# Optimization experiments

Hardware: AMD Instinct MI355X
Metric: run time of the kernel (lower is better)

Reference implementation:

```python
import jax, jax.numpy as jnp
import numpy as np

N_NODES = 100000
N_EDGES = 1600000
N_GRAPHS = 1000


def _gcn_layer(x, W, b, row, col, dinv):
    # GCNConv with improved=True: A_hat = A + 2I, symmetric normalization.
    xw = x @ W  # [N, out]
    norm = dinv[row] * dinv[col]  # [E]
    agg = jax.ops.segment_sum(norm[:, None] * xw[row], col, num_segments=N_NODES)
    # self-loop contribution with fill weight 2.0
    agg = agg + (2.0 * dinv * dinv)[:, None] * xw
    return agg + b


def setup_inputs() -> dict:
    key = jax.random.key(0)
    ks = jax.random.split(key, 20)
    x = jax.random.normal(ks[0], (N_NODES, 336), dtype=jnp.float32)
    edge_index = jax.random.randint(ks[1], (2, N_EDGES), 0, N_NODES, dtype=jnp.int64)
    batch = jnp.sort(jax.random.randint(ks[2], (N_NODES,), 0, N_GRAPHS, dtype=jnp.int64))
    def lin(k, din, dout):
        s = 1.0 / np.sqrt(din)
        return jax.random.uniform(k, (din, dout), jnp.float32, -s, s)
    params = {
        'W1': lin(ks[3], 336, 100), 'b1': jnp.zeros((100,), jnp.float32),
        'W2': lin(ks[4], 100, 100), 'b2': jnp.zeros((100,), jnp.float32),
        'W3': lin(ks[5], 100, 100), 'b3': jnp.zeros((100,), jnp.float32),
        'W4': lin(ks[6], 100, 100), 'b4': jnp.zeros((100,), jnp.float32),
        'W5': lin(ks[7], 100, 100), 'b5': jnp.zeros((100,), jnp.float32),
        'Wl1': lin(ks[8], 100, 100), 'bl1': jnp.zeros((100,), jnp.float32),
        'Wl2': lin(ks[9], 100, 100), 'bl2': jnp.zeros((100,), jnp.float32),
        'Wl3': lin(ks[10], 100, 29), 'bl3': jnp.zeros((29,), jnp.float32),
    }
    return {'x': x, 'edge_index': edge_index, 'batch': batch, **params}


def reference(x, edge_index, batch, W1, b1, W2, b2, W3, b3, W4, b4, W5, b5,
              Wl1, bl1, Wl2, bl2, Wl3, bl3):
    row, col = edge_index[0], edge_index[1]
    # degree of A + 2I (edge weights are 1, self-loop weight 2)
    deg = jax.ops.segment_sum(jnp.ones((N_EDGES,), x.dtype), col, num_segments=N_NODES) + 2.0
    dinv = deg ** -0.5
    h = jax.nn.relu(_gcn_layer(x, W1, b1, row, col, dinv))
    h = jax.nn.relu(_gcn_layer(h, W2, b2, row, col, dinv))
    h = jax.nn.relu(_gcn_layer(h, W3, b3, row, col, dinv))
    h = jax.nn.relu(_gcn_layer(h, W4, b4, row, col, dinv))
    h = jax.nn.relu(_gcn_layer(h, W5, b5, row, col, dinv))
    # global mean pool over graphs
    sums = jax.ops.segment_sum(h, batch, num_segments=N_GRAPHS)
    counts = jax.ops.segment_sum(jnp.ones((N_NODES,), h.dtype), batch, num_segments=N_GRAPHS)
    pooled = sums / jnp.maximum(counts, 1.0)[:, None]
    g = jax.nn.relu(pooled @ Wl1 + bl1)
    g = jax.nn.relu(g @ Wl2 + bl2)
    return g @ Wl3 + bl3
```

## Files before the change

### kernel.cpp

```cpp
#include <hip/hip_runtime.h>
#include <hip/hip_fp16.h>
#include <stdint.h>

#define NN 100000
#define NE 1600000
#define NG 1000
#define LDA 112
#define LDH 112
#define LDX 128

typedef float f32x4 __attribute__((ext_vector_type(4)));
typedef short s16x8 __attribute__((ext_vector_type(8)));

__device__ __forceinline__ unsigned short f2bf(float f) {
    unsigned u = __builtin_bit_cast(unsigned, f);
    unsigned r = u + 0x7FFFu + ((u >> 16) & 1u);
    return (unsigned short)(r >> 16);
}
__device__ __forceinline__ float bf2f(unsigned short h) {
    unsigned u = ((unsigned)h) << 16;
    return __builtin_bit_cast(float, u);
}

__global__ void k_deg(const int* __restrict__ col, int* __restrict__ degcnt) {
    int e = blockIdx.x * 256 + threadIdx.x;
    if (e < NE) atomicAdd(&degcnt[col[e]], 1);
}

__global__ void k_scan1(const int* __restrict__ cnt, int* __restrict__ csum) {
    __shared__ int s[256];
    int i = blockIdx.x * 256 + threadIdx.x;
    s[threadIdx.x] = (i < NN) ? cnt[i] : 0;
    __syncthreads();
    for (int o = 128; o > 0; o >>= 1) {
        if (threadIdx.x < o) s[threadIdx.x] += s[threadIdx.x + o];
        __syncthreads();
    }
    if (threadIdx.x == 0) csum[blockIdx.x] = s[0];
}

__global__ void k_scan2(const int* __restrict__ csum, int* __restrict__ csum2, int nb) {
    __shared__ int s[512];
    int t = threadIdx.x;
    int v = (t < nb) ? csum[t] : 0;
    s[t] = v; __syncthreads();
    for (int o = 1; o < 512; o <<= 1) {
        int x = (t >= o) ? s[t - o] : 0;
        __syncthreads();
        s[t] += x;
        __syncthreads();
    }
    if (t < nb) csum2[t] = s[t] - v;
}

__global__ void k_scan3d(const int* __restrict__ cnt, const int* __restrict__ csum2,
                         int* __restrict__ indptr, float* __restrict__ dinv) {
    __shared__ int s[256];
    int t = threadIdx.x;
    int i = blockIdx.x * 256 + t;
    int v = (i < NN) ? cnt[i] : 0;
    s[t] = v; __syncthreads();
    for (int o = 1; o < 256; o <<= 1) {
        int x = (t >= o) ? s[t - o] : 0;
        __syncthreads();
        s[t] += x;
        __syncthreads();
    }
    if (i < NN) {
        indptr[i] = csum2[blockIdx.x] + s[t] - v;
        dinv[i] = 1.0f / sqrtf((float)v + 2.0f);
    }
    if (i == 0) indptr[NN] = NE;
}

__global__ void k_scatter(const int* __restrict__ row, const int* __restrict__ col,
                          const int* __restrict__ indptr,
                          int* __restrict__ fill, int* __restrict__ esrc) {
    int e = blockIdx.x * 256 + threadIdx.x;
    if (e >= NE) return;
    int r = row[e], c = col[e];
    int pos = indptr[c] + atomicAdd(&fill[c], 1);
    esrc[pos] = r;
}

__global__ void k_gbounds(const int* __restrict__ batch, int* __restrict__ gstart) {
    int i = blockIdx.x * 256 + threadIdx.x;
    if (i >= NN) return;
    int b = batch[i];
    int pb = (i == 0) ? -1 : batch[i - 1];
    for (int g = pb + 1; g <= b; g++) gstart[g] = i;
    if (i == NN - 1) {
        for (int g = b + 1; g <= NG; g++) gstart[g] = NN;
    }
}

__global__ void k_convWall(const float* __restrict__ W1, unsigned short* __restrict__ w1h, unsigned short* __restrict__ w1l,
                           const float* __restrict__ W2, unsigned short* __restrict__ w2h, unsigned short* __restrict__ w2l,
                           const float* __restrict__ W3, unsigned short* __restrict__ w3h, unsigned short* __restrict__ w3l,
                           const float* __restrict__ W4, unsigned short* __restrict__ w4h, unsigned short* __restrict__ w4l,
                           const float* __restrict__ W5, unsigned short* __restrict__ w5h, unsigned short* __restrict__ w5l) {
    int b = blockIdx.x, t = threadIdx.x;
    const float* W; unsigned short *Wh, *Wl; int K, KCP, idx;
    if (b < 168) {
        W = W1; Wh = w1h; Wl = w1l; K = 336; KCP = 384; idx = b * 256 + t;
    } else {
        int li = (b - 168) / 56;
        int lb = (b - 168) % 56;
        const float* Ws[4] = {W2, W3, W4, W5};
        unsigned short* Whs[4] = {w2h, w3h, w4h, w5h};
        unsigned short* Wls[4] = {w2l, w3l, w4l, w5l};
        W = Ws[li]; Wh = Whs[li]; Wl = Wls[li]; K = 100; KCP = 128; idx = lb * 256 + t;
    }
    int n = idx / KCP, k = idx - n * KCP;
    float v = (n < 100 && k < K) ? W[k * 100 + n] : 0.f;
    unsigned short hi = f2bf(v);
    Wh[idx] = hi;
    Wl[idx] = f2bf(v - bf2f(hi));
}

__global__ __launch_bounds__(256) void k_gemm3(const float* __restrict__ A,
                                               const unsigned short* __restrict__ Wthi,
                                               const unsigned short* __restrict__ Wtlo,
                                               const float* __restrict__ dinv,
                                               __half* __restrict__ out,
                                               int M, int K, int KCP, int lda) {
    __shared__ float As[64 * 68];
    __shared__ __align__(16) unsigned short Hs[112 * 72];
    __shared__ __align__(16) unsigned short Ls[112 * 72];
    int t = threadIdx.x;
    int lane = t & 63;
    int wv = t >> 6;
    int l15 = lane & 15, quad = lane >> 4;
    int rowbase = blockIdx.x * 64;

    f32x4 acc[7];
#pragma unroll
    for (int i = 0; i < 7; i++)
#pragma unroll
        for (int r = 0; r < 4; r++) acc[i][r] = 0.f;

    for (int k0 = 0; k0 < KCP; k0 += 64) {
        __syncthreads();
#pragma unroll
        for (int j = 0; j < 4; j++) {
            int e = t + j * 256;
            int r = e >> 4;
            int c4 = (e & 15) * 4;
            int gr = rowbase + r, gk = k0 + c4;
            float4 v = make_float4(0.f, 0.f, 0.f, 0.f);
            if (gr < M && gk < K) v = *(const float4*)(A + (size_t)gr * lda + gk);
            *(float4*)(&As[r * 68 + c4]) = v;
        }
#pragma unroll
        for (int j = 0; j < 7; j++) {
            int e = t + j * 256;
            int n = e >> 4;
            int c = (e & 15) * 4;
            size_t g = (size_t)n * KCP + k0 + c;
            *(uint2*)(&Hs[n * 72 + c]) = *(const uint2*)(Wthi + g);
            *(uint2*)(&Ls[n * 72 + c]) = *(const uint2*)(Wtlo + g);
        }
        __syncthreads();
#pragma unroll
        for (int ks = 0; ks < 2; ks++) {
            int arow = wv * 16 + l15;
            const float* ap = &As[arow * 68 + ks * 32 + quad * 8];
            float4 a0 = *(const float4*)ap;
            float4 a1 = *(const float4*)(ap + 4);
            float af[8] = {a0.x, a0.y, a0.z, a0.w, a1.x, a1.y, a1.z, a1.w};
            s16x8 ahi, alo;
#pragma unroll
            for (int j = 0; j < 8; j++) {
                unsigned short h = f2bf(af[j]);
                ahi[j] = (short)h;
                alo[j] = (short)f2bf(af[j] - bf2f(h));
            }
            int koff = ks * 32 + quad * 8;
#pragma unroll
            for (int tt = 0; tt < 7; tt++) {
                int nrow = tt * 16 + l15;
                s16x8 bhi = *(const s16x8*)(&Hs[nrow * 72 + koff]);
                s16x8 blo = *(const s16x8*)(&Ls[nrow * 72 + koff]);
                acc[tt] = __builtin_amdgcn_mfma_f32_16x16x32_bf16(ahi, bhi, acc[tt], 0, 0, 0);
                acc[tt] = __builtin_amdgcn_mfma_f32_16x16x32_bf16(ahi, blo, acc[tt], 0, 0, 0);
                acc[tt] = __builtin_amdgcn_mfma_f32_16x16x32_bf16(alo, bhi, acc[tt], 0, 0, 0);
            }
        }
    }

    int gr0 = rowbase + wv * 16 + quad * 4;
    float dv[4];
#pragma unroll
    for (int reg = 0; reg < 4; reg++) dv[reg] = (gr0 + reg < M) ? dinv[gr0 + reg] : 0.f;
#pragma unroll
    for (int tt = 0; tt < 7; tt++) {
        int n = tt * 16 + l15;
#pragma unroll
        for (int reg = 0; reg < 4; reg++) {
            int gr = gr0 + reg;
            if (gr < M) out[(size_t)gr * LDX + n] = __float2half(dv[reg] * acc[tt][reg]);
        }
    }
}

__global__ __launch_bounds__(256) void k_gemm3s(const unsigned short* __restrict__ hhi,
                                                const unsigned short* __restrict__ hlo,
                                                const unsigned short* __restrict__ Wthi,
                                                const unsigned short* __restrict__ Wtlo,
                                                const float* __restrict__ dinv,
                                                __half* __restrict__ out) {
    __shared__ __align__(16) unsigned short Ahi[64 * 72];
    __shared__ __align__(16) unsigned short Alo[64 * 72];
    __shared__ __align__(16) unsigned short Hs[112 * 72];
    __shared__ __align__(16) unsigned short Ls[112 * 72];
    int t = threadIdx.x;
    int lane = t & 63;
    int wv = t >> 6;
    int l15 = lane & 15, quad = lane >> 4;
    int rowbase = blockIdx.x * 64;

    f32x4 acc[7];
#pragma unroll
    for (int i = 0; i < 7; i++)
#pragma unroll
        for (int r = 0; r < 4; r++) acc[i][r] = 0.f;

    for (int k0 = 0; k0 < 128; k0 += 64) {
        __syncthreads();
#pragma unroll
        for (int j = 0; j < 2; j++) {
            int e = t + j * 256;
            int r = e >> 3;
            int c8 = (e & 7) * 8;
            int gr = rowbase + r;
            int gk = k0 + c8;
            uint4 vh = make_uint4(0, 0, 0, 0), vl = vh;
            if (gr < NN && gk + 8 <= LDH) {
                size_t g = (size_t)gr * LDH + gk;
                vh = *(const uint4*)(hhi + g);
                vl = *(const uint4*)(hlo + g);
            }
            *(uint4*)(&Ahi[r * 72 + c8]) = vh;
            *(uint4*)(&Alo[r * 72 + c8]) = vl;
        }
#pragma unroll
        for (int j = 0; j < 7; j++) {
            int e = t + j * 256;
            int n = e >> 4;
            int c = (e & 15) * 4;
            size_t g = (size_t)n * 128 + k0 + c;
            *(uint2*)(&Hs[n * 72 + c]) = *(const uint2*)(Wthi + g);
            *(uint2*)(&Ls[n * 72 + c]) = *(const uint2*)(Wtlo + g);
        }
        __syncthreads();
#pragma unroll
        for (int ks = 0; ks < 2; ks++) {
            int arow = wv * 16 + l15;
            int koff = ks * 32 + quad * 8;
            s16x8 ahi = *(const s16x8*)(&Ahi[arow * 72 + koff]);
            s16x8 alo = *(const s16x8*)(&Alo[arow * 72 + koff]);
#pragma unroll
            for (int tt = 0; tt < 7; tt++) {
                int nrow = tt * 16 + l15;
                s16x8 bhi = *(const s16x8*)(&Hs[nrow * 72 + koff]);
                s16x8 blo = *(const s16x8*)(&Ls[nrow * 72 + koff]);
                acc[tt] = __builtin_amdgcn_mfma_f32_16x16x32_bf16(ahi, bhi, acc[tt], 0, 0, 0);
                acc[tt] = __builtin_amdgcn_mfma_f32_16x16x32_bf16(ahi, blo, acc[tt], 0, 0, 0);
                acc[tt] = __builtin_amdgcn_mfma_f32_16x16x32_bf16(alo, bhi, acc[tt], 0, 0, 0);
            }
        }
    }

    int gr0 = rowbase + wv * 16 + quad * 4;
    float dv[4];
#pragma unroll
    for (int reg = 0; reg < 4; reg++) dv[reg] = (gr0 + reg < NN) ? dinv[gr0 + reg] : 0.f;
#pragma unroll
    for (int tt = 0; tt < 7; tt++) {
        int n = tt * 16 + l15;
#pragma unroll
        for (int reg = 0; reg < 4; reg++) {
            int gr = gr0 + reg;
            if (gr < NN) out[(size_t)gr * LDX + n] = __float2half(dv[reg] * acc[tt][reg]);
        }
    }
}

__device__ __forceinline__ void agg_core(const __half* __restrict__ xs,
                                         const int* __restrict__ esrc,
                                         int beg, int end, int lane, int col,
                                         float& ax, float& ay) {
    ax = 0.f; ay = 0.f;
    for (int c = beg; c < end; c += 64) {
        int m = min(64, end - c);
        int se = 0;
        if (lane < m) se = esrc[c + lane];
        int j = 0;
        for (; j + 16 <= m; j += 16) {
            __half2 v[16];
#pragma unroll
            for (int u = 0; u < 16; u++) {
                int s = __builtin_amdgcn_readlane(se, j + u);
                v[u] = *(const __half2*)(xs + (size_t)s * LDX + col);
            }
#pragma unroll
            for (int u = 0; u < 16; u++) {
                float2 f = __half22float2(v[u]);
                ax += f.x; ay += f.y;
            }
        }
        for (; j + 8 <= m; j += 8) {
            __half2 v[8];
#pragma unroll
            for (int u = 0; u < 8; u++) {
                int s = __builtin_amdgcn_readlane(se, j + u);
                v[u] = *(const __half2*)(xs + (size_t)s * LDX + col);
            }
#pragma unroll
            for (int u = 0; u < 8; u++) {
                float2 f = __half22float2(v[u]);
                ax += f.x; ay += f.y;
            }
        }
        for (; j + 4 <= m; j += 4) {
            __half2 v[4];
#pragma unroll
            for (int u = 0; u < 4; u++) {
                int s = __builtin_amdgcn_readlane(se, j + u);
                v[u] = *(const __half2*)(xs + (size_t)s * LDX + col);
            }
#pragma unroll
            for (int u = 0; u < 4; u++) {
                float2 f = __half22float2(v[u]);
                ax += f.x; ay += f.y;
            }
        }
        for (; j < m; j++) {
            int s = __builtin_amdgcn_readlane(se, j);
            float2 f = __half22float2(*(const __half2*)(xs + (size_t)s * LDX + col));
            ax += f.x; ay += f.y;
        }
    }
}

__global__ __launch_bounds__(256) void k_aggS(const __half* __restrict__ xs,
                                              const int* __restrict__ indptr,
                                              const int* __restrict__ esrc,
                                              const float* __restrict__ dinv,
                                              const float* __restrict__ bias,
                                              unsigned short* __restrict__ hhi,
                                              unsigned short* __restrict__ hlo) {
    int wave = threadIdx.x >> 6;
    int lane = threadIdx.x & 63;
    int n = blockIdx.x * 4 + wave;
    if (n >= NN) return;
    int beg = indptr[n], end = indptr[n + 1];
    int col = (lane < 50) ? lane * 2 : 0;
    float ax, ay;
    agg_core(xs, esrc, beg, end, lane, col, ax, ay);
    if (lane < 50) {
        float di = dinv[n];
        float2 xv = __half22float2(*(const __half2*)(xs + (size_t)n * LDX + col));
        float2 bv = *(const float2*)(bias + lane * 2);
        float hx = fmaxf(di * (ax + 2.f * xv.x) + bv.x, 0.f);
        float hy = fmaxf(di * (ay + 2.f * xv.y) + bv.y, 0.f);
        unsigned short xh = f2bf(hx), yh = f2bf(hy);
        *(ushort2*)(hhi + (size_t)n * LDH + col) = make_ushort2(xh, yh);
        *(ushort2*)(hlo + (size_t)n * LDH + col) =
            make_ushort2(f2bf(hx - bf2f(xh)), f2bf(hy - bf2f(yh)));
    } else if (lane < 56) {
        int pc = 100 + (lane - 50) * 2;
        *(ushort2*)(hhi + (size_t)n * LDH + pc) = make_ushort2(0, 0);
        *(ushort2*)(hlo + (size_t)n * LDH + pc) = make_ushort2(0, 0);
    }
}

__global__ __launch_bounds__(256) void k_agg(const __half* __restrict__ xs,
                                             const int* __restrict__ indptr,
                                             const int* __restrict__ esrc,
                                             const float* __restrict__ dinv,
                                             const float* __restrict__ bias,
                                             float* __restrict__ hout) {
    int wave = threadIdx.x >> 6;
    int lane = threadIdx.x & 63;
    int n = blockIdx.x * 4 + wave;
    if (n >= NN) return;
    int beg = indptr[n], end = indptr[n + 1];
    int col = (lane < 50) ? lane * 2 : 0;
    float ax, ay;
    agg_core(xs, esrc, beg, end, lane, col, ax, ay);
    if (lane < 50) {
        float di = dinv[n];
        float2 xv = __half22float2(*(const __half2*)(xs + (size_t)n * LDX + col));
        float2 bv = *(const float2*)(bias + lane * 2);
        float2 r;
        r.x = fmaxf(di * (ax + 2.f * xv.x) + bv.x, 0.f);
        r.y = fmaxf(di * (ay + 2.f * xv.y) + bv.y, 0.f);
        *(float2*)(hout + (size_t)n * LDA + col) = r;
    }
}

__global__ __launch_bounds__(128) void k_pool(const float* __restrict__ h,
                                              const int* __restrict__ gstart,
                                              float* __restrict__ pooled) {
    int g = blockIdx.x, t = threadIdx.x;
    if (t >= 100) return;
    int st = gstart[g];
    int cnt = gstart[g + 1] - st;
    float s0 = 0.f, s1 = 0.f, s2 = 0.f, s3 = 0.f;
    float s4 = 0.f, s5 = 0.f, s6 = 0.f, s7 = 0.f;
    int i = 0;
    for (; i + 8 <= cnt; i += 8) {
        s0 += h[(size_t)(st + i) * LDA + t];
        s1 += h[(size_t)(st + i + 1) * LDA + t];
        s2 += h[(size_t)(st + i + 2) * LDA + t];
        s3 += h[(size_t)(st + i + 3) * LDA + t];
        s4 += h[(size_t)(st + i + 4) * LDA + t];
        s5 += h[(size_t)(st + i + 5) * LDA + t];
        s6 += h[(size_t)(st + i + 6) * LDA + t];
        s7 += h[(size_t)(st + i + 7) * LDA + t];
    }
    for (; i < cnt; i++) s0 += h[(size_t)(st + i) * LDA + t];
    float s = ((s0 + s1) + (s2 + s3)) + ((s4 + s5) + (s6 + s7));
    pooled[g * 100 + t] = s / (float)(cnt > 0 ? cnt : 1);
}

__global__ void k_mlp(const float* __restrict__ pooled,
                      const float* __restrict__ Wl1, const float* __restrict__ bl1,
                      const float* __restrict__ Wl2, const float* __restrict__ bl2,
                      const float* __restrict__ Wl3, const float* __restrict__ bl3,
                      float* __restrict__ out) {
    __shared__ float p[100], q[100];
    int g = blockIdx.x, t = threadIdx.x;
    if (t < 100) p[t] = pooled[g * 100 + t];
    __syncthreads();
    float s1 = 0.f;
    if (t < 100) {
        s1 = bl1[t];
        for (int k = 0; k < 100; k++) s1 += p[k] * Wl1[k * 100 + t];
        s1 = fmaxf(s1, 0.f);
    }
    __syncthreads();
    if (t < 100) q[t] = s1;
    __syncthreads();
    float s2 = 0.f;
    if (t < 100) {
        s2 = bl2[t];
        for (int k = 0; k < 100; k++) s2 += q[k] * Wl2[k * 100 + t];
        s2 = fmaxf(s2, 0.f);
    }
    __syncthreads();
    if (t < 100) p[t] = s2;
    __syncthreads();
    if (t < 29) {
        float s3 = bl3[t];
        for (int k = 0; k < 100; k++) s3 += p[k] * Wl3[k * 29 + t];
        out[g * 29 + t] = s3;
    }
}

extern "C" void kernel_launch(void* const* d_in, const int* in_sizes, int n_in,
                              void* d_out, int out_size, void* d_ws, size_t ws_size,
                              hipStream_t stream) {
    const float* x     = (const float*)d_in[0];
    const int*   ei    = (const int*)d_in[1];
    const int*   batch = (const int*)d_in[2];
    const float* W1 = (const float*)d_in[3];  const float* b1 = (const float*)d_in[4];
    const float* W2 = (const float*)d_in[5];  const float* b2 = (const float*)d_in[6];
    const float* W3 = (const float*)d_in[7];  const float* b3 = (const float*)d_in[8];
    const float* W4 = (const float*)d_in[9];  const float* b4 = (const float*)d_in[10];
    const float* W5 = (const float*)d_in[11]; const float* b5 = (const float*)d_in[12];
    const float* Wl1 = (const float*)d_in[13]; const float* bl1 = (const float*)d_in[14];
    const float* Wl2 = (const float*)d_in[15]; const float* bl2 = (const float*)d_in[16];
    const float* Wl3 = (const float*)d_in[17]; const float* bl3 = (const float*)d_in[18];
    float* out = (float*)d_out;

    const int* row = ei;
    const int* col = ei + NE;

    uintptr_t base = (uintptr_t)d_ws;
    auto alloc = [&](size_t bytes) -> void* {
        void* p = (void*)base;
        base += (bytes + 255) & ~(size_t)255;
        return p;
    };
    int*   cnts   = (int*)alloc((size_t)(2 * NN) * 4);
    int*   degcnt = cnts;
    int*   fill   = cnts + NN;
    float* dinv   = (float*)alloc(NN * 4);
    int*   indptr = (int*)alloc((NN + 1) * 4);
    int*   csum   = (int*)alloc(512 * 4);
    int*   csum2  = (int*)alloc(512 * 4);
    int*   gstart = (int*)alloc((NG + 1) * 4);
    int*   esrc   = (int*)alloc((size_t)NE * 4);
    __half* xsh   = (__half*)alloc((size_t)NN * LDX * 2);
    float* h      = (float*)alloc((size_t)NN * LDA * 4);
    unsigned short* hhi = (unsigned short*)alloc((size_t)NN * LDH * 2);
    unsigned short* hlo = (unsigned short*)alloc((size_t)NN * LDH * 2);
    float* pooled = (float*)alloc((size_t)NG * 100 * 4);
    unsigned short* w1hi = (unsigned short*)alloc((size_t)112 * 384 * 2);
    unsigned short* w1lo = (unsigned short*)alloc((size_t)112 * 384 * 2);
    unsigned short* w2hi = (unsigned short*)alloc((size_t)112 * 128 * 2);
    unsigned short* w2lo = (unsigned short*)alloc((size_t)112 * 128 * 2);
    unsigned short* w3hi = (unsigned short*)alloc((size_t)112 * 128 * 2);
    unsigned short* w3lo = (unsigned short*)alloc((size_t)112 * 128 * 2);
    unsigned short* w4hi = (unsigned short*)alloc((size_t)112 * 128 * 2);
    unsigned short* w4lo = (unsigned short*)alloc((size_t)112 * 128 * 2);
    unsigned short* w5hi = (unsigned short*)alloc((size_t)112 * 128 * 2);
    unsigned short* w5lo = (unsigned short*)alloc((size_t)112 * 128 * 2);

    hipMemsetAsync(cnts, 0, (size_t)(2 * NN) * 4, stream);

    const int NB = (NN + 255) / 256;
    k_deg<<<(NE + 255) / 256, 256, 0, stream>>>(col, degcnt);
    k_scan1<<<NB, 256, 0, stream>>>(degcnt, csum);
    k_scan2<<<1, 512, 0, stream>>>(csum, csum2, NB);
    k_scan3d<<<NB, 256, 0, stream>>>(degcnt, csum2, indptr, dinv);
    k_scatter<<<(NE + 255) / 256, 256, 0, stream>>>(row, col, indptr, fill, esrc);
    k_gbounds<<<NB, 256, 0, stream>>>(batch, gstart);
    k_convWall<<<392, 256, 0, stream>>>(W1, w1hi, w1lo, W2, w2hi, w2lo,
                                        W3, w3hi, w3lo, W4, w4hi, w4lo,
                                        W5, w5hi, w5lo);

    const int GEMM_GRID = (NN + 63) / 64;
    const int AGG_GRID = (NN + 3) / 4;

    k_gemm3<<<GEMM_GRID, 256, 0, stream>>>(x, w1hi, w1lo, dinv, xsh, NN, 336, 384, 336);
    k_aggS<<<AGG_GRID, 256, 0, stream>>>(xsh, indptr, esrc, dinv, b1, hhi, hlo);
    k_gemm3s<<<GEMM_GRID, 256, 0, stream>>>(hhi, hlo, w2hi, w2lo, dinv, xsh);
    k_aggS<<<AGG_GRID, 256, 0, stream>>>(xsh, indptr, esrc, dinv, b2, hhi, hlo);
    k_gemm3s<<<GEMM_GRID, 256, 0, stream>>>(hhi, hlo, w3hi, w3lo, dinv, xsh);
    k_aggS<<<AGG_GRID, 256, 0, stream>>>(xsh, indptr, esrc, dinv, b3, hhi, hlo);
    k_gemm3s<<<GEMM_GRID, 256, 0, stream>>>(hhi, hlo, w4hi, w4lo, dinv, xsh);
    k_aggS<<<AGG_GRID, 256, 0, stream>>>(xsh, indptr, esrc, dinv, b4, hhi, hlo);
    k_gemm3s<<<GEMM_GRID, 256, 0, stream>>>(hhi, hlo, w5hi, w5lo, dinv, xsh);
    k_agg<<<AGG_GRID, 256, 0, stream>>>(xsh, indptr, esrc, dinv, b5, h);

    k_pool<<<NG, 128, 0, stream>>>(h, gstart, pooled);
    k_mlp<<<NG, 128, 0, stream>>>(pooled, Wl1, bl1, Wl2, bl2, Wl3, bl3, out);
}
```

Before: 879.1 us.

## Switch GEMMs to fp16 activations with split fp16 weights and async LDS loads

Replaces the bf16 hi/lo three-MFMA split with fp16 activations times fp16 hi/lo weights, using two MFMAs per tile with the low part scaled by 2048. Intermediate activations are stored as a single fp16 buffer instead of two bf16 buffers, which halves activation traffic. Tiles are loaded into swizzled LDS through global_load_lds, and layer 1 uses larger K steps of 128. Rounding activations to fp16 lowers precision and can overflow for large values.

```diff
diff --git a/kernel.cpp b/kernel.cpp
--- a/kernel.cpp
+++ b/kernel.cpp
@@ -6,20 +6,15 @@
 #define NE 1600000
 #define NG 1000
 #define LDA 112
-#define LDH 112
 #define LDX 128
 
 typedef float f32x4 __attribute__((ext_vector_type(4)));
-typedef short s16x8 __attribute__((ext_vector_type(8)));
-
-__device__ __forceinline__ unsigned short f2bf(float f) {
-    unsigned u = __builtin_bit_cast(unsigned, f);
-    unsigned r = u + 0x7FFFu + ((u >> 16) & 1u);
-    return (unsigned short)(r >> 16);
-}
-__device__ __forceinline__ float bf2f(unsigned short h) {
-    unsigned u = ((unsigned)h) << 16;
-    return __builtin_bit_cast(float, u);
+typedef _Float16 f16x8 __attribute__((ext_vector_type(8)));
+
+__device__ __forceinline__ void load_lds16(const void* g, void* l) {
+    __builtin_amdgcn_global_load_lds((const __attribute__((address_space(1))) unsigned int*)g,
+                                     (__attribute__((address_space(3))) unsigned int*)l,
+                                     16, 0, 0);
 }
 
 __global__ void k_deg(const int* __restrict__ col, int* __restrict__ degcnt) {
@@ -94,96 +89,99 @@
     }
 }
 
-__global__ void k_convWall(const float* __restrict__ W1, unsigned short* __restrict__ w1h, unsigned short* __restrict__ w1l,
-                           const float* __restrict__ W2, unsigned short* __restrict__ w2h, unsigned short* __restrict__ w2l,
-                           const float* __restrict__ W3, unsigned short* __restrict__ w3h, unsigned short* __restrict__ w3l,
-                           const float* __restrict__ W4, unsigned short* __restrict__ w4h, unsigned short* __restrict__ w4l,
-                           const float* __restrict__ W5, unsigned short* __restrict__ w5h, unsigned short* __restrict__ w5l) {
+__global__ void k_convW(const float* __restrict__ W1, __half* __restrict__ w1h, __half* __restrict__ w1l,
+                        const float* __restrict__ W2, __half* __restrict__ w2h, __half* __restrict__ w2l,
+                        const float* __restrict__ W3, __half* __restrict__ w3h, __half* __restrict__ w3l,
+                        const float* __restrict__ W4, __half* __restrict__ w4h, __half* __restrict__ w4l,
+                        const float* __restrict__ W5, __half* __restrict__ w5h, __half* __restrict__ w5l) {
     int b = blockIdx.x, t = threadIdx.x;
-    const float* W; unsigned short *Wh, *Wl; int K, KCP, idx;
+    const float* W; __half *Wh, *Wl; int K, KCP, idx;
     if (b < 168) {
         W = W1; Wh = w1h; Wl = w1l; K = 336; KCP = 384; idx = b * 256 + t;
     } else {
         int li = (b - 168) / 56;
         int lb = (b - 168) % 56;
         const float* Ws[4] = {W2, W3, W4, W5};
-        unsigned short* Whs[4] = {w2h, w3h, w4h, w5h};
-        unsigned short* Wls[4] = {w2l, w3l, w4l, w5l};
+        __half* Whs[4] = {w2h, w3h, w4h, w5h};
+        __half* Wls[4] = {w2l, w3l, w4l, w5l};
         W = Ws[li]; Wh = Whs[li]; Wl = Wls[li]; K = 100; KCP = 128; idx = lb * 256 + t;
     }
     int n = idx / KCP, k = idx - n * KCP;
     float v = (n < 100 && k < K) ? W[k * 100 + n] : 0.f;
-    unsigned short hi = f2bf(v);
+    __half hi = __float2half(v);
     Wh[idx] = hi;
-    Wl[idx] = f2bf(v - bf2f(hi));
-}
-
-__global__ __launch_bounds__(256) void k_gemm3(const float* __restrict__ A,
-                                               const unsigned short* __restrict__ Wthi,
-                                               const unsigned short* __restrict__ Wtlo,
+    Wl[idx] = __float2half((v - __half2float(hi)) * 2048.f);
+}
+
+__global__ __launch_bounds__(256) void k_gemmX(const float* __restrict__ x,
+                                               const __half* __restrict__ Whi,
+                                               const __half* __restrict__ Wlo,
                                                const float* __restrict__ dinv,
-                                               __half* __restrict__ out,
-                                               int M, int K, int KCP, int lda) {
-    __shared__ float As[64 * 68];
-    __shared__ __align__(16) unsigned short Hs[112 * 72];
-    __shared__ __align__(16) unsigned short Ls[112 * 72];
+                                               __half* __restrict__ out) {
+    __shared__ __align__(16) __half Ah[64 * 128];
+    __shared__ __align__(16) __half Hs[112 * 128];
+    __shared__ __align__(16) __half Ls[112 * 128];
     int t = threadIdx.x;
-    int lane = t & 63;
-    int wv = t >> 6;
+    int lane = t & 63, wv = t >> 6;
     int l15 = lane & 15, quad = lane >> 4;
     int rowbase = blockIdx.x * 64;
 
-    f32x4 acc[7];
+    f32x4 acch[7], accl[7];
 #pragma unroll
     for (int i = 0; i < 7; i++)
 #pragma unroll
-        for (int r = 0; r < 4; r++) acc[i][r] = 0.f;
-
-    for (int k0 = 0; k0 < KCP; k0 += 64) {
-        __syncthreads();
+        for (int r = 0; r < 4; r++) { acch[i][r] = 0.f; accl[i][r] = 0.f; }
+
+    for (int k0 = 0; k0 < 384; k0 += 128) {
+        __syncthreads();
+#pragma unroll
+        for (int j = 0; j < 7; j++) {
+            int o = (t + j * 256) * 16;
+            int r = o >> 8;
+            int scb = (o & 255) ^ ((r & 7) << 4);
+            size_t goff = (size_t)r * 768 + (size_t)k0 * 2 + scb;
+            load_lds16((const char*)Whi + goff, (char*)Hs + o);
+            load_lds16((const char*)Wlo + goff, (char*)Ls + o);
+        }
 #pragma unroll
         for (int j = 0; j < 4; j++) {
-            int e = t + j * 256;
-            int r = e >> 4;
-            int c4 = (e & 15) * 4;
-            int gr = rowbase + r, gk = k0 + c4;
-            float4 v = make_float4(0.f, 0.f, 0.f, 0.f);
-            if (gr < M && gk < K) v = *(const float4*)(A + (size_t)gr * lda + gk);
-            *(float4*)(&As[r * 68 + c4]) = v;
-        }
-#pragma unroll
-        for (int j = 0; j < 7; j++) {
-            int e = t + j * 256;
-            int n = e >> 4;
-            int c = (e & 15) * 4;
-            size_t g = (size_t)n * KCP + k0 + c;
-            *(uint2*)(&Hs[n * 72 + c]) = *(const uint2*)(Wthi + g);
-            *(uint2*)(&Ls[n * 72 + c]) = *(const uint2*)(Wtlo + g);
-        }
-        __syncthreads();
-#pragma unroll
-        for (int ks = 0; ks < 2; ks++) {
-            int arow = wv * 16 + l15;
-            const float* ap = &As[arow * 68 + ks * 32 + quad * 8];
-            float4 a0 = *(const float4*)ap;
-            float4 a1 = *(const float4*)(ap + 4);
-            float af[8] = {a0.x, a0.y, a0.z, a0.w, a1.x, a1.y, a1.z, a1.w};
-            s16x8 ahi, alo;
-#pragma unroll
-            for (int j = 0; j < 8; j++) {
-                unsigned short h = f2bf(af[j]);
-                ahi[j] = (short)h;
-                alo[j] = (short)f2bf(af[j] - bf2f(h));
-            }
-            int koff = ks * 32 + quad * 8;
+            int i = t + j * 256;
+            int r = i >> 4;
+            int o = i * 16;
+            int sc = (o & 255) ^ ((r & 7) << 4);
+            int rowg = rowbase + r;
+            int k = k0 + (sc >> 1);
+            float4 v0 = make_float4(0.f, 0.f, 0.f, 0.f), v1 = v0;
+            if (rowg < NN && k < 336) {
+                const float* p = x + (size_t)rowg * 336 + k;
+                v0 = *(const float4*)p;
+                v1 = *(const float4*)(p + 4);
+            }
+            __half2 p0 = __floats2half2_rn(v0.x, v0.y);
+            __half2 p1 = __floats2half2_rn(v0.z, v0.w);
+            __half2 p2 = __floats2half2_rn(v1.x, v1.y);
+            __half2 p3 = __floats2half2_rn(v1.z, v1.w);
+            uint4 pk;
+            pk.x = __builtin_bit_cast(unsigned, p0);
+            pk.y = __builtin_bit_cast(unsigned, p1);
+            pk.z = __builtin_bit_cast(unsigned, p2);
+            pk.w = __builtin_bit_cast(unsigned, p3);
+            *(uint4*)((char*)Ah + o) = pk;
+        }
+        __syncthreads();
+        int swz = (l15 & 7) << 4;
+        const char* abase = (const char*)Ah + (wv * 16 + l15) * 256;
+#pragma unroll
+        for (int ks = 0; ks < 4; ks++) {
+            int cb = (ks * 64 + quad * 16) ^ swz;
+            f16x8 a = *(const f16x8*)(abase + cb);
 #pragma unroll
             for (int tt = 0; tt < 7; tt++) {
                 int nrow = tt * 16 + l15;
-                s16x8 bhi = *(const s16x8*)(&Hs[nrow * 72 + koff]);
-                s16x8 blo = *(const s16x8*)(&Ls[nrow * 72 + koff]);
-                acc[tt] = __builtin_amdgcn_mfma_f32_16x16x32_bf16(ahi, bhi, acc[tt], 0, 0, 0);
-                acc[tt] = __builtin_amdgcn_mfma_f32_16x16x32_bf16(ahi, blo, acc[tt], 0, 0, 0);
-                acc[tt] = __builtin_amdgcn_mfma_f32_16x16x32_bf16(alo, bhi, acc[tt], 0, 0, 0);
+                f16x8 bh = *(const f16x8*)((const char*)Hs + nrow * 256 + cb);
+                f16x8 bl = *(const f16x8*)((const char*)Ls + nrow * 256 + cb);
+                acch[tt] = __builtin_amdgcn_mfma_f32_16x16x32_f16(a, bh, acch[tt], 0, 0, 0);
+                accl[tt] = __builtin_amdgcn_mfma_f32_16x16x32_f16(a, bl, accl[tt], 0, 0, 0);
             }
         }
     }
@@ -191,83 +189,77 @@
     int gr0 = rowbase + wv * 16 + quad * 4;
     float dv[4];
 #pragma unroll
-    for (int reg = 0; reg < 4; reg++) dv[reg] = (gr0 + reg < M) ? dinv[gr0 + reg] : 0.f;
+    for (int reg = 0; reg < 4; reg++) dv[reg] = (gr0 + reg < NN) ? dinv[gr0 + reg] : 0.f;
 #pragma unroll
     for (int tt = 0; tt < 7; tt++) {
         int n = tt * 16 + l15;
 #pragma unroll
         for (int reg = 0; reg < 4; reg++) {
             int gr = gr0 + reg;
-            if (gr < M) out[(size_t)gr * LDX + n] = __float2half(dv[reg] * acc[tt][reg]);
-        }
-    }
-}
-
-__global__ __launch_bounds__(256) void k_gemm3s(const unsigned short* __restrict__ hhi,
-                                                const unsigned short* __restrict__ hlo,
-                                                const unsigned short* __restrict__ Wthi,
-                                                const unsigned short* __restrict__ Wtlo,
-                                                const float* __restrict__ dinv,
-                                                __half* __restrict__ out) {
-    __shared__ __align__(16) unsigned short Ahi[64 * 72];
-    __shared__ __align__(16) unsigned short Alo[64 * 72];
-    __shared__ __align__(16) unsigned short Hs[112 * 72];
-    __shared__ __align__(16) unsigned short Ls[112 * 72];
+            if (gr < NN)
+                out[(size_t)gr * LDX + n] =
+                    __float2half(dv[reg] * (acch[tt][reg] + accl[tt][reg] * (1.f / 2048.f)));
+        }
+    }
+    if (l15 < 8) {
+#pragma unroll
+        for (int reg = 0; reg < 4; reg++) {
+            int gr = gr0 + reg;
+            if (gr < NN) *(unsigned int*)(out + (size_t)gr * LDX + 112 + l15 * 2) = 0u;
+        }
+    }
+}
+
+__global__ __launch_bounds__(256) void k_gemmH(const __half* __restrict__ act,
+                                               const __half* __restrict__ Whi,
+                                               const __half* __restrict__ Wlo,
+                                               const float* __restrict__ dinv,
+                                               __half* __restrict__ out) {
+    __shared__ __align__(16) __half Ah[64 * 128];
+    __shared__ __align__(16) __half Hs[112 * 128];
+    __shared__ __align__(16) __half Ls[112 * 128];
     int t = threadIdx.x;
-    int lane = t & 63;
-    int wv = t >> 6;
+    int lane = t & 63, wv = t >> 6;
     int l15 = lane & 15, quad = lane >> 4;
     int rowbase = blockIdx.x * 64;
 
-    f32x4 acc[7];
+#pragma unroll
+    for (int j = 0; j < 4; j++) {
+        int o = (t + j * 256) * 16;
+        int r = o >> 8;
+        int scb = (o & 255) ^ ((r & 7) << 4);
+        load_lds16((const char*)act + (size_t)(rowbase + r) * 256 + scb, (char*)Ah + o);
+    }
+#pragma unroll
+    for (int j = 0; j < 7; j++) {
+        int o = (t + j * 256) * 16;
+        int r = o >> 8;
+        int scb = (o & 255) ^ ((r & 7) << 4);
+        size_t goff = (size_t)r * 256 + scb;
+        load_lds16((const char*)Whi + goff, (char*)Hs + o);
+        load_lds16((const char*)Wlo + goff, (char*)Ls + o);
+    }
+
+    f32x4 acch[7], accl[7];
 #pragma unroll
     for (int i = 0; i < 7; i++)
 #pragma unroll
-        for (int r = 0; r < 4; r++) acc[i][r] = 0.f;
-
-    for (int k0 = 0; k0 < 128; k0 += 64) {
-        __syncthreads();
-#pragma unroll
-        for (int j = 0; j < 2; j++) {
-            int e = t + j * 256;
-            int r = e >> 3;
-            int c8 = (e & 7) * 8;
-            int gr = rowbase + r;
-            int gk = k0 + c8;
-            uint4 vh = make_uint4(0, 0, 0, 0), vl = vh;
-            if (gr < NN && gk + 8 <= LDH) {
-                size_t g = (size_t)gr * LDH + gk;
-                vh = *(const uint4*)(hhi + g);
-                vl = *(const uint4*)(hlo + g);
-            }
-            *(uint4*)(&Ahi[r * 72 + c8]) = vh;
-            *(uint4*)(&Alo[r * 72 + c8]) = vl;
-        }
-#pragma unroll
-        for (int j = 0; j < 7; j++) {
-            int e = t + j * 256;
-            int n = e >> 4;
-            int c = (e & 15) * 4;
-            size_t g = (size_t)n * 128 + k0 + c;
-            *(uint2*)(&Hs[n * 72 + c]) = *(const uint2*)(Wthi + g);
-            *(uint2*)(&Ls[n * 72 + c]) = *(const uint2*)(Wtlo + g);
-        }
-        __syncthreads();
-#pragma unroll
-        for (int ks = 0; ks < 2; ks++) {
-            int arow = wv * 16 + l15;
-            int koff = ks * 32 + quad * 8;
-            s16x8 ahi = *(const s16x8*)(&Ahi[arow * 72 + koff]);
-            s16x8 alo = *(const s16x8*)(&Alo[arow * 72 + koff]);
-#pragma unroll
-            for (int tt = 0; tt < 7; tt++) {
-                int nrow = tt * 16 + l15;
-                s16x8 bhi = *(const s16x8*)(&Hs[nrow * 72 + koff]);
-                s16x8 blo = *(const s16x8*)(&Ls[nrow * 72 + koff]);
-                acc[tt] = __builtin_amdgcn_mfma_f32_16x16x32_bf16(ahi, bhi, acc[tt], 0, 0, 0);
-                acc[tt] = __builtin_amdgcn_mfma_f32_16x16x32_bf16(ahi, blo, acc[tt], 0, 0, 0);
-                acc[tt] = __builtin_amdgcn_mfma_f32_16x16x32_bf16(alo, bhi, acc[tt], 0, 0, 0);
-            }
+        for (int r = 0; r < 4; r++) { acch[i][r] = 0.f; accl[i][r] = 0.f; }
+
+    __syncthreads();
+    int swz = (l15 & 7) << 4;
+    const char* abase = (const char*)Ah + (wv * 16 + l15) * 256;
+#pragma unroll
+    for (int ks = 0; ks < 4; ks++) {
+        int cb = (ks * 64 + quad * 16) ^ swz;
+        f16x8 a = *(const f16x8*)(abase + cb);
+#pragma unroll
+        for (int tt = 0; tt < 7; tt++) {
+            int nrow = tt * 16 + l15;
+            f16x8 bh = *(const f16x8*)((const char*)Hs + nrow * 256 + cb);
+            f16x8 bl = *(const f16x8*)((const char*)Ls + nrow * 256 + cb);
+            acch[tt] = __builtin_amdgcn_mfma_f32_16x16x32_f16(a, bh, acch[tt], 0, 0, 0);
+            accl[tt] = __builtin_amdgcn_mfma_f32_16x16x32_f16(a, bl, accl[tt], 0, 0, 0);
         }
     }
 
@@ -281,7 +273,16 @@
 #pragma unroll
         for (int reg = 0; reg < 4; reg++) {
             int gr = gr0 + reg;
-            if (gr < NN) out[(size_t)gr * LDX + n] = __float2half(dv[reg] * acc[tt][reg]);
+            if (gr < NN)
+                out[(size_t)gr * LDX + n] =
+                    __float2half(dv[reg] * (acch[tt][reg] + accl[tt][reg] * (1.f / 2048.f)));
+        }
+    }
+    if (l15 < 8) {
+#pragma unroll
+        for (int reg = 0; reg < 4; reg++) {
+            int gr = gr0 + reg;
+            if (gr < NN) *(unsigned int*)(out + (size_t)gr * LDX + 112 + l15 * 2) = 0u;
         }
     }
 }
@@ -348,8 +349,7 @@
                                               const int* __restrict__ esrc,
                                               const float* __restrict__ dinv,
                                               const float* __restrict__ bias,
-                                              unsigned short* __restrict__ hhi,
-                                              unsigned short* __restrict__ hlo) {
+                                              __half* __restrict__ hh) {
     int wave = threadIdx.x >> 6;
     int lane = threadIdx.x & 63;
     int n = blockIdx.x * 4 + wave;
@@ -364,14 +364,10 @@
         float2 bv = *(const float2*)(bias + lane * 2);
         float hx = fmaxf(di * (ax + 2.f * xv.x) + bv.x, 0.f);
         float hy = fmaxf(di * (ay + 2.f * xv.y) + bv.y, 0.f);
-        unsigned short xh = f2bf(hx), yh = f2bf(hy);
-        *(ushort2*)(hhi + (size_t)n * LDH + col) = make_ushort2(xh, yh);
-        *(ushort2*)(hlo + (size_t)n * LDH + col) =
-            make_ushort2(f2bf(hx - bf2f(xh)), f2bf(hy - bf2f(yh)));
-    } else if (lane < 56) {
+        *(__half2*)(hh + (size_t)n * LDX + col) = __floats2half2_rn(hx, hy);
+    } else {
         int pc = 100 + (lane - 50) * 2;
-        *(ushort2*)(hhi + (size_t)n * LDH + pc) = make_ushort2(0, 0);
-        *(ushort2*)(hlo + (size_t)n * LDH + pc) = make_ushort2(0, 0);
+        *(unsigned int*)(hh + (size_t)n * LDX + pc) = 0u;
     }
 }
 
@@ -493,21 +489,20 @@
     int*   csum2  = (int*)alloc(512 * 4);
     int*   gstart = (int*)alloc((NG + 1) * 4);
     int*   esrc   = (int*)alloc((size_t)NE * 4);
-    __half* xsh   = (__half*)alloc((size_t)NN * LDX * 2);
+    __half* xsh   = (__half*)alloc((size_t)NN * LDX * 2 + 8192);
+    __half* hh    = (__half*)alloc((size_t)NN * LDX * 2 + 8192);
     float* h      = (float*)alloc((size_t)NN * LDA * 4);
-    unsigned short* hhi = (unsigned short*)alloc((size_t)NN * LDH * 2);
-    unsigned short* hlo = (unsigned short*)alloc((size_t)NN * LDH * 2);
     float* pooled = (float*)alloc((size_t)NG * 100 * 4);
-    unsigned short* w1hi = (unsigned short*)alloc((size_t)112 * 384 * 2);
-    unsigned short* w1lo = (unsigned short*)alloc((size_t)112 * 384 * 2);
-    unsigned short* w2hi = (unsigned short*)alloc((size_t)112 * 128 * 2);
-    unsigned short* w2lo = (unsigned short*)alloc((size_t)112 * 128 * 2);
-    unsigned short* w3hi = (unsigned short*)alloc((size_t)112 * 128 * 2);
-    unsigned short* w3lo = (unsigned short*)alloc((size_t)112 * 128 * 2);
-    unsigned short* w4hi = (unsigned short*)alloc((size_t)112 * 128 * 2);
-    unsigned short* w4lo = (unsigned short*)alloc((size_t)112 * 128 * 2);
-    unsigned short* w5hi = (unsigned short*)alloc((size_t)112 * 128 * 2);
-    unsigned short* w5lo = (unsigned short*)alloc((size_t)112 * 128 * 2);
+    __half* w1hi = (__half*)alloc((size_t)112 * 384 * 2);
+    __half* w1lo = (__half*)alloc((size_t)112 * 384 * 2);
+    __half* w2hi = (__half*)alloc((size_t)112 * 128 * 2);
+    __half* w2lo = (__half*)alloc((size_t)112 * 128 * 2);
+    __half* w3hi = (__half*)alloc((size_t)112 * 128 * 2);
+    __half* w3lo = (__half*)alloc((size_t)112 * 128 * 2);
+    __half* w4hi = (__half*)alloc((size_t)112 * 128 * 2);
+    __half* w4lo = (__half*)alloc((size_t)112 * 128 * 2);
+    __half* w5hi = (__half*)alloc((size_t)112 * 128 * 2);
+    __half* w5lo = (__half*)alloc((size_t)112 * 128 * 2);
 
     hipMemsetAsync(cnts, 0, (size_t)(2 * NN) * 4, stream);
 
@@ -518,22 +513,22 @@
     k_scan3d<<<NB, 256, 0, stream>>>(degcnt, csum2, indptr, dinv);
     k_scatter<<<(NE + 255) / 256, 256, 0, stream>>>(row, col, indptr, fill, esrc);
     k_gbounds<<<NB, 256, 0, stream>>>(batch, gstart);
-    k_convWall<<<392, 256, 0, stream>>>(W1, w1hi, w1lo, W2, w2hi, w2lo,
-                                        W3, w3hi, w3lo, W4, w4hi, w4lo,
-                                        W5, w5hi, w5lo);
+    k_convW<<<392, 256, 0, stream>>>(W1, w1hi, w1lo, W2, w2hi, w2lo,
+                                     W3, w3hi, w3lo, W4, w4hi, w4lo,
+                                     W5, w5hi, w5lo);
 
     const int GEMM_GRID = (NN + 63) / 64;
     const int AGG_GRID = (NN + 3) / 4;
 
-    k_gemm3<<<GEMM_GRID, 256, 0, stream>>>(x, w1hi, w1lo, dinv, xsh, NN, 336, 384, 336);
-    k_aggS<<<AGG_GRID, 256, 0, stream>>>(xsh, indptr, esrc, dinv, b1, hhi, hlo);
-    k_gemm3s<<<GEMM_GRID, 256, 0, stream>>>(hhi, hlo, w2hi, w2lo, dinv, xsh);
-    k_aggS<<<AGG_GRID, 256, 0, stream>>>(xsh, indptr, esrc, dinv, b2, hhi, hlo);
-    k_gemm3s<<<GEMM_GRID, 256, 0, stream>>>(hhi, hlo, w3hi, w3lo, dinv, xsh);
-    k_aggS<<<AGG_GRID, 256, 0, stream>>>(xsh, indptr, esrc, dinv, b3, hhi, hlo);
-    k_gemm3s<<<GEMM_GRID, 256, 0, stream>>>(hhi, hlo, w4hi, w4lo, dinv, xsh);
-    k_aggS<<<AGG_GRID, 256, 0, stream>>>(xsh, indptr, esrc, dinv, b4, hhi, hlo);
-    k_gemm3s<<<GEMM_GRID, 256, 0, stream>>>(hhi, hlo, w5hi, w5lo, dinv, xsh);
+    k_gemmX<<<GEMM_GRID, 256, 0, stream>>>(x, w1hi, w1lo, dinv, xsh);
+    k_aggS<<<AGG_GRID, 256, 0, stream>>>(xsh, indptr, esrc, dinv, b1, hh);
+    k_gemmH<<<GEMM_GRID, 256, 0, stream>>>(hh, w2hi, w2lo, dinv, xsh);
+    k_aggS<<<AGG_GRID, 256, 0, stream>>>(xsh, indptr, esrc, dinv, b2, hh);
+    k_gemmH<<<GEMM_GRID, 256, 0, stream>>>(hh, w3hi, w3lo, dinv, xsh);
+    k_aggS<<<AGG_GRID, 256, 0, stream>>>(xsh, indptr, esrc, dinv, b3, hh);
+    k_gemmH<<<GEMM_GRID, 256, 0, stream>>>(hh, w4hi, w4lo, dinv, xsh);
+    k_aggS<<<AGG_GRID, 256, 0, stream>>>(xsh, indptr, esrc, dinv, b4, hh);
+    k_gemmH<<<GEMM_GRID, 256, 0, stream>>>(hh, w5hi, w5lo, dinv, xsh);
     k_agg<<<AGG_GRID, 256, 0, stream>>>(xsh, indptr, esrc, dinv, b5, h);
 
     k_pool<<<NG, 128, 0, stream>>>(h, gstart, pooled);
```

Result: slower. 908.6 us (+3.4%).
